# Kernel tuning notes

Hardware: AMD Instinct MI355X
Metric: run time of the kernel (lower is better)

## Reference

```python
import jax, jax.numpy as jnp
import numpy as np

EMBED_DIM = 1024
N_TOKENS = 8192


def setup_inputs() -> dict:
    key = jax.random.key(0)
    k1, k2, k3 = jax.random.split(key, 3)
    inputs = jax.random.normal(k1, (N_TOKENS, EMBED_DIM), dtype=jnp.float32)
    rotation_params = jax.random.normal(k2, (EMBED_DIM, EMBED_DIM), dtype=jnp.float32)
    entangle_params = jax.random.normal(k3, (EMBED_DIM, EMBED_DIM), dtype=jnp.float32)
    return {"inputs": inputs, "rotation_params": rotation_params, "entangle_params": entangle_params}


def reference(inputs, rotation_params, entangle_params):
    # query/key projections from externally supplied params
    embed_dim = inputs.shape[-1]
    wq = rotation_params.reshape(embed_dim, -1)
    wk = entangle_params.reshape(embed_dim, -1)
    query = inputs @ wq          # [N, d]
    key = inputs @ wk            # [N, d]
    scale = 1.0 / jnp.sqrt(jnp.float32(embed_dim))
    scores = jax.nn.softmax(jnp.einsum('nd,md->nm', query, key) * scale, axis=-1)  # [N, N]
    context = scores @ inputs    # attend over raw inputs (V = inputs)
    return context
```

## Files before the change

kernel.cpp:

```cpp
#include <hip/hip_runtime.h>
#include <hip/hip_bf16.h>


typedef _Float16 f16x8 __attribute__((ext_vector_type(8)));
typedef _Float16 f16x4 __attribute__((ext_vector_type(4)));
typedef float    f32x4 __attribute__((ext_vector_type(4)));

#define TM 128
#define TN 128

__device__ __forceinline__ void g2lds16(const _Float16* g, _Float16* l) {
    __builtin_amdgcn_global_load_lds(
        (__attribute__((address_space(1))) unsigned int*)(g),
        (__attribute__((address_space(3))) unsigned int*)(l),
        16, 0, 0);
}


__global__ void prep_x(const float* __restrict__ src,
                       _Float16* __restrict__ hi, _Float16* __restrict__ lo,
                       _Float16* __restrict__ xt, int R, int C) {
    __shared__ float tile[32][33];
    int c0 = blockIdx.x * 32, r0 = blockIdx.y * 32;
    int tx = threadIdx.x, ty = threadIdx.y;
#pragma unroll
    for (int k = 0; k < 4; ++k) {
        int r = ty + 8 * k;
        size_t idx = (size_t)(r0 + r) * C + c0 + tx;
        float v = src[idx];
        tile[r][tx] = v;
        _Float16 h = (_Float16)v;
        hi[idx] = h;
        lo[idx] = (_Float16)(v - (float)h);
    }
    __syncthreads();
#pragma unroll
    for (int k = 0; k < 4; ++k) {
        float v = tile[tx][ty + 8 * k];
        xt[(size_t)(c0 + ty + 8 * k) * R + r0 + tx] = (_Float16)v;
    }
}

__global__ void transpose_split(const float* __restrict__ src,
                                _Float16* __restrict__ dhi,
                                _Float16* __restrict__ dlo,
                                int R, int C) {
    __shared__ float tile[32][33];
    int c0 = blockIdx.x * 32, r0 = blockIdx.y * 32;
    int tx = threadIdx.x, ty = threadIdx.y;
#pragma unroll
    for (int k = 0; k < 4; ++k)
        tile[ty + 8 * k][tx] = src[(size_t)(r0 + ty + 8 * k) * C + c0 + tx];
    __syncthreads();
#pragma unroll
    for (int k = 0; k < 4; ++k) {
        float v = tile[tx][ty + 8 * k];
        _Float16 h = (_Float16)v;
        size_t idx = (size_t)(c0 + ty + 8 * k) * R + r0 + tx;
        dhi[idx] = h;
        dlo[idx] = (_Float16)(v - (float)h);
    }
}

__global__ __launch_bounds__(256) void add_rows(const float* __restrict__ a,
                                                const float* __restrict__ b,
                                                float* __restrict__ out, long n4) {
    long i = (long)blockIdx.x * blockDim.x + threadIdx.x;
    long stride = (long)gridDim.x * blockDim.x;
    for (; i < n4; i += stride) {
        float4 x = ((const float4*)a)[i];
        float4 y = ((const float4*)b)[i];
        x.x += y.x; x.y += y.y; x.z += y.z; x.w += y.w;
        ((float4*)out)[i] = x;
    }
}

template <int TERMS, int SPLIT_OUT, int SWAP, int BKH>
__global__ __launch_bounds__(256, 4) void gemm_bt(
    const _Float16* __restrict__ Ahi, const _Float16* __restrict__ Alo,
    const _Float16* __restrict__ Bhi, const _Float16* __restrict__ Blo,
    float* __restrict__ C, _Float16* __restrict__ Chi, _Float16* __restrict__ Clo,
    long lda, long ldb, long ldc, int K, long zA, long zB, long zC) {
    constexpr int NBUF = (TERMS == 3) ? 4 : 2;
    __shared__ __align__(16) _Float16 s[NBUF * 128 * BKH];

    const long z = blockIdx.z;
    Ahi += z * zA;
    Bhi += z * zB;
    if constexpr (TERMS == 3) { Alo += z * zA; Blo += z * zB; }
    if constexpr (SPLIT_OUT) { Chi += z * zC; Clo += z * zC; }
    else C += z * zC;

    const int t = threadIdx.x;
    const int wave = t >> 6;
    const int lane = t & 63;
    const int lm = lane & 15;
    const int lq = lane >> 4;
    const int wr = wave >> 1;
    const int wc = wave & 1;

    const long rowBase = (long)(SWAP ? blockIdx.x : blockIdx.y) * TM;
    const long colBase = (long)(SWAP ? blockIdx.y : blockIdx.x) * TN;

    const _Float16* src;
    long myLd, gRow0;
    int ldsBaseH;
    if constexpr (TERMS == 3) {
        const _Float16* a = (wave & 1) ? Alo : Ahi;
        const _Float16* b = (wave & 1) ? Blo : Bhi;
        src = (wave & 2) ? b : a;
        myLd = (wave & 2) ? ldb : lda;
        gRow0 = (wave & 2) ? colBase : rowBase;
        ldsBaseH = wave * (128 * BKH);
    } else {
        src = (wave & 2) ? Bhi : Ahi;
        myLd = (wave & 2) ? ldb : lda;
        gRow0 = ((wave & 2) ? colBase : rowBase) + (wave & 1) * 64;
        ldsBaseH = (wave >> 1) * (128 * BKH) + (wave & 1) * (64 * BKH);
    }
    constexpr int LPR = BKH / 8;
    constexpr int RPI = 64 / LPR;
    constexpr int NISS = (TERMS == 3 ? 128 : 64) / RPI;
    const int lr = lane / LPR;
    const int slot = lane % LPR;
    const int swzW = (BKH == 32) ? ((lr >> 1) & 3) : (lr & 7);
    const _Float16* rp = src + (gRow0 + lr) * myLd + (slot ^ swzW) * 8;
    _Float16* ldsW = &s[ldsBaseH];

    const _Float16* sAh = s;
    const _Float16* sBh = s + (TERMS == 3 ? 2 : 1) * 128 * BKH;
    const _Float16* sAl = s + 128 * BKH;
    const _Float16* sBl = s + 3 * 128 * BKH;

    const int swzR = (BKH == 32) ? ((lm >> 1) & 3) : (lm & 7);

    f32x4 acc[4][4];
#pragma unroll
    for (int r = 0; r < 4; ++r)
#pragma unroll
        for (int c = 0; c < 4; ++c)
#pragma unroll
            for (int i = 0; i < 4; ++i) acc[r][c][i] = 0.0f;

    for (int k0 = 0; k0 < K; k0 += BKH) {
        __syncthreads();
#pragma unroll
        for (int j = 0; j < NISS; ++j)
            g2lds16(rp + (long)(j * RPI) * myLd + k0, ldsW + j * 512);
        __syncthreads();

#pragma unroll
        for (int kk = 0; kk < BKH; kk += 32) {
            const int gb = kk >> 3;
            f16x8 ah[4], bh[4], al[4], bl[4];
#pragma unroll
            for (int r = 0; r < 4; ++r) {
                int ra = (wr * 64 + r * 16 + lm) * BKH + ((gb + lq) ^ swzR) * 8;
                int rb = (wc * 64 + r * 16 + lm) * BKH + ((gb + lq) ^ swzR) * 8;
                ah[r] = *(const f16x8*)&sAh[ra];
                bh[r] = *(const f16x8*)&sBh[rb];
                if constexpr (TERMS == 3) {
                    al[r] = *(const f16x8*)&sAl[ra];
                    bl[r] = *(const f16x8*)&sBl[rb];
                }
            }
#pragma unroll
            for (int r = 0; r < 4; ++r)
#pragma unroll
                for (int c = 0; c < 4; ++c) {
                    acc[r][c] = __builtin_amdgcn_mfma_f32_16x16x32_f16(
                        ah[r], bh[c], acc[r][c], 0, 0, 0);
                    if constexpr (TERMS == 3) {
                        acc[r][c] = __builtin_amdgcn_mfma_f32_16x16x32_f16(
                            ah[r], bl[c], acc[r][c], 0, 0, 0);
                        acc[r][c] = __builtin_amdgcn_mfma_f32_16x16x32_f16(
                            al[r], bh[c], acc[r][c], 0, 0, 0);
                    }
                }
        }
    }

#pragma unroll
    for (int r = 0; r < 4; ++r)
#pragma unroll
        for (int c = 0; c < 4; ++c)
#pragma unroll
            for (int i = 0; i < 4; ++i) {
                long row = rowBase + wr * 64 + r * 16 + lq * 4 + i;
                long col = colBase + wc * 64 + c * 16 + lm;
                if constexpr (SPLIT_OUT) {
                    float v = acc[r][c][i];
                    _Float16 h = (_Float16)v;
                    Chi[row * ldc + col] = h;
                    Clo[row * ldc + col] = (_Float16)(v - (float)h);
                } else {
                    C[row * ldc + col] = acc[r][c][i];
                }
            }
}

__global__ __launch_bounds__(256) void softmax_rows(const float* __restrict__ S,
                                                    _Float16* __restrict__ P,
                                                    long ldp, int N) {
    const int row = blockIdx.x;
    const int t = threadIdx.x;
    const float4* rowp = (const float4*)(S + (size_t)row * N);
    float4 v[8];
    float mx = -3.4e38f;
#pragma unroll
    for (int g = 0; g < 4; ++g) {
        v[2 * g]     = rowp[2 * t + 512 * g];
        v[2 * g + 1] = rowp[2 * t + 512 * g + 1];
    }
#pragma unroll
    for (int i = 0; i < 8; ++i)
        mx = fmaxf(mx, fmaxf(fmaxf(v[i].x, v[i].y), fmaxf(v[i].z, v[i].w)));
    __shared__ float red[8];
#pragma unroll
    for (int off = 32; off >= 1; off >>= 1) mx = fmaxf(mx, __shfl_xor(mx, off));
    if ((t & 63) == 0) red[t >> 6] = mx;
    __syncthreads();
    mx = fmaxf(fmaxf(red[0], red[1]), fmaxf(red[2], red[3]));

    float sum = 0.0f;
#pragma unroll
    for (int i = 0; i < 8; ++i) {
        v[i].x = __expf((v[i].x - mx) * 0.03125f);
        v[i].y = __expf((v[i].y - mx) * 0.03125f);
        v[i].z = __expf((v[i].z - mx) * 0.03125f);
        v[i].w = __expf((v[i].w - mx) * 0.03125f);
        sum += (v[i].x + v[i].y) + (v[i].z + v[i].w);
    }
#pragma unroll
    for (int off = 32; off >= 1; off >>= 1) sum += __shfl_xor(sum, off);
    if ((t & 63) == 0) red[4 + (t >> 6)] = sum;
    __syncthreads();
    float inv = 1.0f / (red[4] + red[5] + red[6] + red[7]);

    f16x8* prow = (f16x8*)(P + (size_t)row * ldp);
#pragma unroll
    for (int g = 0; g < 4; ++g) {
        float4 a = v[2 * g], b = v[2 * g + 1];
        f16x8 o;
        o[0] = (_Float16)(a.x * inv); o[1] = (_Float16)(a.y * inv);
        o[2] = (_Float16)(a.z * inv); o[3] = (_Float16)(a.w * inv);
        o[4] = (_Float16)(b.x * inv); o[5] = (_Float16)(b.y * inv);
        o[6] = (_Float16)(b.z * inv); o[7] = (_Float16)(b.w * inv);
        prow[t + 256 * g] = o;
    }
}

extern "C" void kernel_launch(void* const* d_in, const int* in_sizes, int n_in,
                              void* d_out, int out_size, void* d_ws, size_t ws_size,
                              hipStream_t stream) {
    const float* X  = (const float*)d_in[0];
    const float* Wq = (const float*)d_in[1];
    const float* Wk = (const float*)d_in[2];
    float* out = (float*)d_out;

    const long Nt = 8192, D = 1024;
    char* ws = (char*)d_ws;
    const size_t MB = 1024ull * 1024ull;

    _Float16* XT  = (_Float16*)(ws + 0);
    _Float16* Qhi = (_Float16*)(ws + 16 * MB);
    _Float16* Qlo = (_Float16*)(ws + 32 * MB);
    _Float16* Khi = (_Float16*)(ws + 48 * MB);
    _Float16* Klo = (_Float16*)(ws + 64 * MB);
    _Float16* Xhi   = (_Float16*)(ws + 80 * MB);
    _Float16* Xlo   = (_Float16*)(ws + 96 * MB);
    _Float16* WqThi = (_Float16*)(ws + 112 * MB);
    _Float16* WqTlo = (_Float16*)(ws + 114 * MB);
    _Float16* WkThi = (_Float16*)(ws + 116 * MB);
    _Float16* WkTlo = (_Float16*)(ws + 118 * MB);
    float* PK0 = (float*)(ws + 16 * MB);

    const size_t rowBytes = (size_t)Nt * 4;
    const bool planA = ws_size >= 208 * MB + 128 * rowBytes;
    _Float16* Pbuf = (_Float16*)(ws + 80 * MB);
    float* Sc;
    long chunk;
    if (planA) {
        Sc = (float*)(ws + 208 * MB);
        size_t avail = ws_size - 208 * MB;
        chunk = (long)((avail / rowBytes / 128) * 128);
    } else {
        Sc = (float*)(ws + 80 * MB);
        size_t avail = ws_size > 80 * MB ? ws_size - 80 * MB : 0;
        chunk = (long)((avail / rowBytes / 128) * 128);
        if (chunk < 128) chunk = 128;
    }
    if (chunk > Nt) chunk = Nt;
    {
        long nch = (Nt + chunk - 1) / chunk;
        chunk = (((Nt + nch - 1) / nch) + 127) / 128 * 128;
    }

    prep_x<<<dim3(32, 256), dim3(32, 8), 0, stream>>>(X, Xhi, Xlo, XT,
                                                      (int)Nt, (int)D);
    transpose_split<<<dim3(32, 32), dim3(32, 8), 0, stream>>>(Wq, WqThi, WqTlo,
                                                              (int)D, (int)D);
    transpose_split<<<dim3(32, 32), dim3(32, 8), 0, stream>>>(Wk, WkThi, WkTlo,
                                                              (int)D, (int)D);

    gemm_bt<3, 1, 1, 32><<<dim3(Nt / TM, D / TN, 2), 256, 0, stream>>>(
        Xhi, Xlo, WqThi, WqTlo, nullptr, Qhi, Qlo, D, D, D, (int)D,
        0, (long)(4 * MB / 2), (long)(32 * MB / 2));

    long done = 0;
    while (done < Nt) {
        long cur = Nt - done < chunk ? Nt - done : chunk;
        gemm_bt<3, 0, 0, 32><<<dim3(Nt / TN, cur / TM, 1), 256, 0, stream>>>(
            Qhi + done * D, Qlo + done * D, Khi, Klo, Sc, nullptr, nullptr,
            D, D, Nt, (int)D, 0, 0, 0);
        if (planA) {
            softmax_rows<<<(int)cur, 256, 0, stream>>>(Sc, Pbuf + done * Nt,
                                                       Nt, (int)Nt);
        } else {
            softmax_rows<<<(int)cur, 256, 0, stream>>>(Sc, (_Float16*)Sc,
                                                       2 * Nt, (int)Nt);
            gemm_bt<1, 0, 1, 64><<<dim3(cur / TM, D / TN, 1), 256, 0, stream>>>(
                (const _Float16*)Sc, nullptr, XT, nullptr,
                out + done * D, nullptr, nullptr, 2 * Nt, Nt, D, (int)Nt,
                0, 0, 0);
        }
        done += cur;
    }

    if (planA) {
        gemm_bt<1, 0, 1, 64><<<dim3(Nt / TM, D / TN, 2), 256, 0, stream>>>(
            Pbuf, nullptr, XT, nullptr, PK0, nullptr, nullptr,
            Nt, Nt, D, (int)(Nt / 2),
            Nt / 2, Nt / 2, Nt * D);
        add_rows<<<1024, 256, 0, stream>>>(PK0, PK0 + Nt * D, out, Nt * D / 4);
    }
}
```

Before: 830.5 us.

## Replace GEMM with 256x256-tile double-buffered kernel and XCD-aware block remap

Replaces the 128x128, 256-thread GEMM with a 256x256-tile, 512-thread kernel. The new kernel double-buffers LDS so the global-to-LDS load for the next K tile overlaps the MFMAs on the current one. It also splits each K step into four phases with barriers and setprio hints, and remaps block IDs so consecutive tiles land on the same XCD for L2 reuse. The aim is to remove the load/compute serialization and raise data reuse per tile, at the cost of more LDS and registers (two blocks per CU) and fewer blocks in the grid.

```diff
diff --git a/kernel.cpp b/kernel.cpp
--- a/kernel.cpp
+++ b/kernel.cpp
@@ -3,11 +3,7 @@
 
 
 typedef _Float16 f16x8 __attribute__((ext_vector_type(8)));
-typedef _Float16 f16x4 __attribute__((ext_vector_type(4)));
 typedef float    f32x4 __attribute__((ext_vector_type(4)));
-
-#define TM 128
-#define TN 128
 
 __device__ __forceinline__ void g2lds16(const _Float16* g, _Float16* l) {
     __builtin_amdgcn_global_load_lds(
@@ -75,126 +71,166 @@
     }
 }
 
-template <int TERMS, int SPLIT_OUT, int SWAP, int BKH>
-__global__ __launch_bounds__(256, 4) void gemm_bt(
+template <int TERMS, int BKH, int SWAP, int SPLIT_OUT>
+__global__ __launch_bounds__(512, 2) void gemm_p4(
     const _Float16* __restrict__ Ahi, const _Float16* __restrict__ Alo,
     const _Float16* __restrict__ Bhi, const _Float16* __restrict__ Blo,
     float* __restrict__ C, _Float16* __restrict__ Chi, _Float16* __restrict__ Clo,
-    long lda, long ldb, long ldc, int K, long zA, long zB, long zC) {
-    constexpr int NBUF = (TERMS == 3) ? 4 : 2;
-    __shared__ __align__(16) _Float16 s[NBUF * 128 * BKH];
+    long lda, long ldb, long ldc, int K, int nrb, int ncb,
+    long zA, long zB, long zC) {
+    static_assert(BKH == 32 || BKH == 64, "");
+    constexpr int NMAT = (TERMS == 3) ? 4 : 2;
+    constexpr int KK   = BKH / 32;
+    constexpr int LPR  = BKH / 8;
+    constexpr int RPI  = 512 / LPR;
+    constexpr int IPM  = 256 / RPI;
+    constexpr int MATH = 256 * BKH;
+    __shared__ __align__(16) _Float16 s[2][NMAT * MATH];
 
     const long z = blockIdx.z;
-    Ahi += z * zA;
-    Bhi += z * zB;
+    Ahi += z * zA; Bhi += z * zB;
     if constexpr (TERMS == 3) { Alo += z * zA; Blo += z * zB; }
     if constexpr (SPLIT_OUT) { Chi += z * zC; Clo += z * zC; }
     else C += z * zC;
+
+    const int nb = nrb * ncb;
+    const int orig = blockIdx.x;
+    const int q = nb >> 3, r8 = nb & 7;
+    const int xcd = orig & 7, pos = orig >> 3;
+    const int sw = (xcd < r8 ? xcd * (q + 1) : r8 * (q + 1) + (xcd - r8) * q) + pos;
+    int rb, cb;
+    if constexpr (SWAP) { rb = sw / ncb; cb = sw % ncb; }
+    else                { cb = sw / nrb; rb = sw % nrb; }
+    const long rowBase = (long)rb * 256;
+    const long colBase = (long)cb * 256;
 
     const int t = threadIdx.x;
     const int wave = t >> 6;
     const int lane = t & 63;
     const int lm = lane & 15;
     const int lq = lane >> 4;
-    const int wr = wave >> 1;
-    const int wc = wave & 1;
-
-    const long rowBase = (long)(SWAP ? blockIdx.x : blockIdx.y) * TM;
-    const long colBase = (long)(SWAP ? blockIdx.y : blockIdx.x) * TN;
-
-    const _Float16* src;
-    long myLd, gRow0;
-    int ldsBaseH;
+    const int wr = wave >> 2;
+    const int wc = wave & 3;
+
+    const int row0 = t / LPR;
+    const int slot = t % LPR;
+    const int swzW = (BKH == 32) ? ((row0 >> 1) & 3) : (row0 & 7);
+    const _Float16* gsrc[NMAT];
+    long gld[NMAT];
+    gsrc[0] = Ahi + (rowBase + row0) * lda + (slot ^ swzW) * 8; gld[0] = lda;
     if constexpr (TERMS == 3) {
-        const _Float16* a = (wave & 1) ? Alo : Ahi;
-        const _Float16* b = (wave & 1) ? Blo : Bhi;
-        src = (wave & 2) ? b : a;
-        myLd = (wave & 2) ? ldb : lda;
-        gRow0 = (wave & 2) ? colBase : rowBase;
-        ldsBaseH = wave * (128 * BKH);
+        gsrc[1] = Alo + (rowBase + row0) * lda + (slot ^ swzW) * 8; gld[1] = lda;
+        gsrc[2] = Bhi + (colBase + row0) * ldb + (slot ^ swzW) * 8; gld[2] = ldb;
+        gsrc[3] = Blo + (colBase + row0) * ldb + (slot ^ swzW) * 8; gld[3] = ldb;
     } else {
-        src = (wave & 2) ? Bhi : Ahi;
-        myLd = (wave & 2) ? ldb : lda;
-        gRow0 = ((wave & 2) ? colBase : rowBase) + (wave & 1) * 64;
-        ldsBaseH = (wave >> 1) * (128 * BKH) + (wave & 1) * (64 * BKH);
-    }
-    constexpr int LPR = BKH / 8;
-    constexpr int RPI = 64 / LPR;
-    constexpr int NISS = (TERMS == 3 ? 128 : 64) / RPI;
-    const int lr = lane / LPR;
-    const int slot = lane % LPR;
-    const int swzW = (BKH == 32) ? ((lr >> 1) & 3) : (lr & 7);
-    const _Float16* rp = src + (gRow0 + lr) * myLd + (slot ^ swzW) * 8;
-    _Float16* ldsW = &s[ldsBaseH];
-
-    const _Float16* sAh = s;
-    const _Float16* sBh = s + (TERMS == 3 ? 2 : 1) * 128 * BKH;
-    const _Float16* sAl = s + 128 * BKH;
-    const _Float16* sBl = s + 3 * 128 * BKH;
+        gsrc[1] = Bhi + (colBase + row0) * ldb + (slot ^ swzW) * 8; gld[1] = ldb;
+    }
+    const int ldsRow = wave * (64 / LPR);
 
     const int swzR = (BKH == 32) ? ((lm >> 1) & 3) : (lm & 7);
 
-    f32x4 acc[4][4];
-#pragma unroll
-    for (int r = 0; r < 4; ++r)
-#pragma unroll
-        for (int c = 0; c < 4; ++c)
-#pragma unroll
-            for (int i = 0; i < 4; ++i) acc[r][c][i] = 0.0f;
-
-    for (int k0 = 0; k0 < K; k0 += BKH) {
-        __syncthreads();
-#pragma unroll
-        for (int j = 0; j < NISS; ++j)
-            g2lds16(rp + (long)(j * RPI) * myLd + k0, ldsW + j * 512);
-        __syncthreads();
-
-#pragma unroll
-        for (int kk = 0; kk < BKH; kk += 32) {
-            const int gb = kk >> 3;
-            f16x8 ah[4], bh[4], al[4], bl[4];
-#pragma unroll
-            for (int r = 0; r < 4; ++r) {
-                int ra = (wr * 64 + r * 16 + lm) * BKH + ((gb + lq) ^ swzR) * 8;
-                int rb = (wc * 64 + r * 16 + lm) * BKH + ((gb + lq) ^ swzR) * 8;
-                ah[r] = *(const f16x8*)&sAh[ra];
-                bh[r] = *(const f16x8*)&sBh[rb];
-                if constexpr (TERMS == 3) {
-                    al[r] = *(const f16x8*)&sAl[ra];
-                    bl[r] = *(const f16x8*)&sBl[rb];
+    f32x4 acc[8][4];
+#pragma unroll
+    for (int rr = 0; rr < 8; ++rr)
+#pragma unroll
+        for (int cc = 0; cc < 4; ++cc)
+#pragma unroll
+            for (int i = 0; i < 4; ++i) acc[rr][cc][i] = 0.0f;
+
+    const int NT = K / BKH;
+    int cur = 0;
+
+#pragma unroll
+    for (int m = 0; m < NMAT; ++m)
+#pragma unroll
+        for (int j = 0; j < IPM; ++j)
+            g2lds16(gsrc[m] + (long)(j * RPI) * gld[m],
+                    &s[0][m * MATH + (j * RPI + ldsRow) * BKH]);
+    __syncthreads();
+
+    for (int tt = 0; tt < NT; ++tt) {
+        const _Float16* sAh = &s[cur][0];
+        const _Float16* sAl = sAh + MATH;
+        const _Float16* sBh = sAh + (TERMS == 3 ? 2 : 1) * MATH;
+        const _Float16* sBl = sAh + 3 * MATH;
+        f16x8 bh[4 * KK], bl[TERMS == 3 ? 4 * KK : 1];
+#pragma unroll
+        for (int p = 0; p < 4; ++p) {
+            if (p == 0 && tt + 1 < NT) {
+                const long k0 = (long)(tt + 1) * BKH;
+#pragma unroll
+                for (int m = 0; m < NMAT; ++m)
+#pragma unroll
+                    for (int j = 0; j < IPM; ++j)
+                        g2lds16(gsrc[m] + (long)(j * RPI) * gld[m] + k0,
+                                &s[cur ^ 1][m * MATH + (j * RPI + ldsRow) * BKH]);
+            }
+            f16x8 ah[2 * KK], al[TERMS == 3 ? 2 * KK : 1];
+#pragma unroll
+            for (int rr = 0; rr < 2; ++rr) {
+                const int arow = wr * 128 + (2 * p + rr) * 16 + lm;
+#pragma unroll
+                for (int kk = 0; kk < KK; ++kk) {
+                    const int off = arow * BKH + (((kk * 4 + lq) ^ swzR) << 3);
+                    ah[rr * KK + kk] = *(const f16x8*)&sAh[off];
+                    if constexpr (TERMS == 3)
+                        al[rr * KK + kk] = *(const f16x8*)&sAl[off];
                 }
             }
-#pragma unroll
-            for (int r = 0; r < 4; ++r)
-#pragma unroll
-                for (int c = 0; c < 4; ++c) {
-                    acc[r][c] = __builtin_amdgcn_mfma_f32_16x16x32_f16(
-                        ah[r], bh[c], acc[r][c], 0, 0, 0);
-                    if constexpr (TERMS == 3) {
-                        acc[r][c] = __builtin_amdgcn_mfma_f32_16x16x32_f16(
-                            ah[r], bl[c], acc[r][c], 0, 0, 0);
-                        acc[r][c] = __builtin_amdgcn_mfma_f32_16x16x32_f16(
-                            al[r], bh[c], acc[r][c], 0, 0, 0);
+            if (p == 0) {
+#pragma unroll
+                for (int cc = 0; cc < 4; ++cc) {
+                    const int brow = wc * 64 + cc * 16 + lm;
+#pragma unroll
+                    for (int kk = 0; kk < KK; ++kk) {
+                        const int off = brow * BKH + (((kk * 4 + lq) ^ swzR) << 3);
+                        bh[cc * KK + kk] = *(const f16x8*)&sBh[off];
+                        if constexpr (TERMS == 3)
+                            bl[cc * KK + kk] = *(const f16x8*)&sBl[off];
                     }
                 }
+            }
+            __builtin_amdgcn_s_barrier();
+            asm volatile("s_waitcnt lgkmcnt(0)" ::: "memory");
+            __builtin_amdgcn_sched_barrier(0);
+            __builtin_amdgcn_s_setprio(1);
+#pragma unroll
+            for (int rr = 0; rr < 2; ++rr)
+#pragma unroll
+                for (int cc = 0; cc < 4; ++cc)
+#pragma unroll
+                    for (int kk = 0; kk < KK; ++kk) {
+                        acc[2 * p + rr][cc] = __builtin_amdgcn_mfma_f32_16x16x32_f16(
+                            ah[rr * KK + kk], bh[cc * KK + kk], acc[2 * p + rr][cc], 0, 0, 0);
+                        if constexpr (TERMS == 3) {
+                            acc[2 * p + rr][cc] = __builtin_amdgcn_mfma_f32_16x16x32_f16(
+                                ah[rr * KK + kk], bl[cc * KK + kk], acc[2 * p + rr][cc], 0, 0, 0);
+                            acc[2 * p + rr][cc] = __builtin_amdgcn_mfma_f32_16x16x32_f16(
+                                al[rr * KK + kk], bh[cc * KK + kk], acc[2 * p + rr][cc], 0, 0, 0);
+                        }
+                    }
+            __builtin_amdgcn_s_setprio(0);
+            if (p < 3) __builtin_amdgcn_s_barrier();
         }
-    }
-
-#pragma unroll
-    for (int r = 0; r < 4; ++r)
-#pragma unroll
-        for (int c = 0; c < 4; ++c)
+        __syncthreads();
+        cur ^= 1;
+    }
+
+#pragma unroll
+    for (int rr = 0; rr < 8; ++rr)
+#pragma unroll
+        for (int cc = 0; cc < 4; ++cc)
 #pragma unroll
             for (int i = 0; i < 4; ++i) {
-                long row = rowBase + wr * 64 + r * 16 + lq * 4 + i;
-                long col = colBase + wc * 64 + c * 16 + lm;
+                const long row = rowBase + wr * 128 + rr * 16 + lq * 4 + i;
+                const long col = colBase + wc * 64 + cc * 16 + lm;
                 if constexpr (SPLIT_OUT) {
-                    float v = acc[r][c][i];
+                    float v = acc[rr][cc][i];
                     _Float16 h = (_Float16)v;
                     Chi[row * ldc + col] = h;
                     Clo[row * ldc + col] = (_Float16)(v - (float)h);
                 } else {
-                    C[row * ldc + col] = acc[r][c][i];
+                    C[row * ldc + col] = acc[rr][cc][i];
                 }
             }
 }
@@ -276,24 +312,24 @@
     float* PK0 = (float*)(ws + 16 * MB);
 
     const size_t rowBytes = (size_t)Nt * 4;
-    const bool planA = ws_size >= 208 * MB + 128 * rowBytes;
+    const bool planA = ws_size >= 208 * MB + 256 * rowBytes;
     _Float16* Pbuf = (_Float16*)(ws + 80 * MB);
     float* Sc;
     long chunk;
     if (planA) {
         Sc = (float*)(ws + 208 * MB);
         size_t avail = ws_size - 208 * MB;
-        chunk = (long)((avail / rowBytes / 128) * 128);
+        chunk = (long)((avail / rowBytes / 256) * 256);
     } else {
         Sc = (float*)(ws + 80 * MB);
         size_t avail = ws_size > 80 * MB ? ws_size - 80 * MB : 0;
-        chunk = (long)((avail / rowBytes / 128) * 128);
-        if (chunk < 128) chunk = 128;
+        chunk = (long)((avail / rowBytes / 256) * 256);
+        if (chunk < 256) chunk = 256;
     }
     if (chunk > Nt) chunk = Nt;
     {
         long nch = (Nt + chunk - 1) / chunk;
-        chunk = (((Nt + nch - 1) / nch) + 127) / 128 * 128;
+        chunk = (((Nt + nch - 1) / nch) + 255) / 256 * 256;
     }
 
     prep_x<<<dim3(32, 256), dim3(32, 8), 0, stream>>>(X, Xhi, Xlo, XT,
@@ -303,34 +339,36 @@
     transpose_split<<<dim3(32, 32), dim3(32, 8), 0, stream>>>(Wk, WkThi, WkTlo,
                                                               (int)D, (int)D);
 
-    gemm_bt<3, 1, 1, 32><<<dim3(Nt / TM, D / TN, 2), 256, 0, stream>>>(
-        Xhi, Xlo, WqThi, WqTlo, nullptr, Qhi, Qlo, D, D, D, (int)D,
+    gemm_p4<3, 32, 1, 1><<<dim3(32 * 4, 1, 2), 512, 0, stream>>>(
+        Xhi, Xlo, WqThi, WqTlo, nullptr, Qhi, Qlo,
+        D, D, D, (int)D, 32, 4,
         0, (long)(4 * MB / 2), (long)(32 * MB / 2));
 
     long done = 0;
     while (done < Nt) {
         long cur = Nt - done < chunk ? Nt - done : chunk;
-        gemm_bt<3, 0, 0, 32><<<dim3(Nt / TN, cur / TM, 1), 256, 0, stream>>>(
+        int nrb = (int)(cur / 256), ncb = (int)(Nt / 256);
+        gemm_p4<3, 32, 1, 0><<<dim3(nrb * ncb, 1, 1), 512, 0, stream>>>(
             Qhi + done * D, Qlo + done * D, Khi, Klo, Sc, nullptr, nullptr,
-            D, D, Nt, (int)D, 0, 0, 0);
+            D, D, Nt, (int)D, nrb, ncb, 0, 0, 0);
         if (planA) {
             softmax_rows<<<(int)cur, 256, 0, stream>>>(Sc, Pbuf + done * Nt,
                                                        Nt, (int)Nt);
         } else {
             softmax_rows<<<(int)cur, 256, 0, stream>>>(Sc, (_Float16*)Sc,
                                                        2 * Nt, (int)Nt);
-            gemm_bt<1, 0, 1, 64><<<dim3(cur / TM, D / TN, 1), 256, 0, stream>>>(
+            gemm_p4<1, 64, 0, 0><<<dim3((int)(cur / 256) * 4, 1, 1), 512, 0, stream>>>(
                 (const _Float16*)Sc, nullptr, XT, nullptr,
-                out + done * D, nullptr, nullptr, 2 * Nt, Nt, D, (int)Nt,
-                0, 0, 0);
+                out + done * D, nullptr, nullptr,
+                2 * Nt, Nt, D, (int)Nt, (int)(cur / 256), 4, 0, 0, 0);
         }
         done += cur;
     }
 
     if (planA) {
-        gemm_bt<1, 0, 1, 64><<<dim3(Nt / TM, D / TN, 2), 256, 0, stream>>>(
+        gemm_p4<1, 64, 0, 0><<<dim3(32 * 4, 1, 2), 512, 0, stream>>>(
             Pbuf, nullptr, XT, nullptr, PK0, nullptr, nullptr,
-            Nt, Nt, D, (int)(Nt / 2),
+            Nt, Nt, D, (int)(Nt / 2), 32, 4,
             Nt / 2, Nt / 2, Nt * D);
         add_rows<<<1024, 256, 0, stream>>>(PK0, PK0 + Nt * D, out, Nt * D / 4);
     }
```

Result: slower. 877.4 us (+5.6%).
